# Kernel tuning notes

Hardware: AMD Instinct MI355X
Metric: run time of the kernel (lower is better)

The kernel has to match this reference:

```python
import jax, jax.numpy as jnp
import numpy as np

NUM_CONTEXT = 8  # context panels; +1 choice -> 9 panels, 72 ordered pairs (i != j)

_PAIRS = np.array([(i, j) for i in range(9) for j in range(9) if i != j], dtype=np.int32)
I_IDX = jnp.asarray(_PAIRS[:, 0])  # [72]
J_IDX = jnp.asarray(_PAIRS[:, 1])  # [72]


def setup_inputs() -> dict:
    key = jax.random.key(0)
    ks = jax.random.split(key, 10)
    B, C, F, H = 256, 8, 512, 256
    s_in = 1.0 / np.sqrt(2 * F)
    s_h = 1.0 / np.sqrt(H)
    return {
        "context_features": jax.random.normal(ks[0], (B, NUM_CONTEXT, F), jnp.float32),
        "choice_features": jax.random.normal(ks[1], (B, C, F), jnp.float32),
        "W1": jax.random.uniform(ks[2], (2 * F, H), jnp.float32, -s_in, s_in),
        "b1": jax.random.uniform(ks[3], (H,), jnp.float32, -s_in, s_in),
        "W2": jax.random.uniform(ks[4], (H, H), jnp.float32, -s_h, s_h),
        "b2": jax.random.uniform(ks[5], (H,), jnp.float32, -s_h, s_h),
        "W3": jax.random.uniform(ks[6], (H, H), jnp.float32, -s_h, s_h),
        "b3": jax.random.uniform(ks[7], (H,), jnp.float32, -s_h, s_h),
        "W4": jax.random.uniform(ks[8], (H, 1), jnp.float32, -s_h, s_h),
        "b4": jax.random.uniform(ks[9], (1,), jnp.float32, -s_h, s_h),
    }


def reference(context_features, choice_features, W1, b1, W2, b2, W3, b3, W4, b4):
    B, C, F = choice_features.shape[0], choice_features.shape[1], choice_features.shape[2]
    # panels[b, c, p, f]: 8 context panels + 1 choice panel per candidate choice
    ctx = jnp.broadcast_to(context_features[:, None, :, :], (B, C, NUM_CONTEXT, F))
    panels = jnp.concatenate([ctx, choice_features[:, :, None, :]], axis=2)  # [B,C,9,F]
    # all 72 ordered pairs (i != j), concatenated features -> [B,C,72,2F]
    pair = jnp.concatenate([panels[:, :, I_IDX, :], panels[:, :, J_IDX, :]], axis=-1)
    # g_theta MLP
    h = jax.nn.relu(pair @ W1 + b1)
    h = jax.nn.relu(h @ W2 + b2)        # [B,C,72,H]
    agg = h.mean(axis=2)                # [B,C,H]
    # f_phi MLP (dropout is identity in eval mode)
    g = jax.nn.relu(agg @ W3 + b3)
    score = g @ W4 + b4                 # [B,C,1]
    return score[..., 0]                # [B,C]
```

## Files before the change

kernel.cpp:

```cpp
#include <hip/hip_runtime.h>
#include <hip/hip_bf16.h>


typedef __bf16 bf16_t;
typedef bf16_t bf16x8 __attribute__((ext_vector_type(8)));
typedef bf16_t bf16x4 __attribute__((ext_vector_type(4)));
typedef float f32x4 __attribute__((ext_vector_type(4)));

#define MFMA16(a, b, c) __builtin_amdgcn_mfma_f32_16x16x32_bf16((a), (b), (c), 0, 0, 0)

__global__ __launch_bounds__(256) void prep_kernel(
    const float* __restrict__ W1, const float* __restrict__ W2,
    const float* __restrict__ W3, bf16_t* __restrict__ Wp,
    bf16_t* __restrict__ W2T, bf16_t* __restrict__ W3T) {
  __shared__ float Ts[64][65];
  const int b = blockIdx.x;
  const int t = threadIdx.x;
  const int r = t >> 6;
  const int c = t & 63;
  const float* srcP;
  bf16_t* dstP;
  int srcRow, srcCol, dr0, dc0, dstride;
  if (b < 64) {
    const int k0 = (b >> 3) * 64, j0 = (b & 7) * 64;
    srcP = W1; dstP = Wp; dstride = 512;
    srcRow = (j0 < 256) ? k0 : 512 + k0;
    srcCol = (j0 < 256) ? j0 : j0 - 256;
    dr0 = j0; dc0 = k0;
  } else if (b < 80) {
    const int s = b - 64;
    const int k0 = (s >> 2) * 64, n0 = (s & 3) * 64;
    srcP = W2; dstP = W2T; dstride = 256;
    srcRow = k0; srcCol = n0; dr0 = n0; dc0 = k0;
  } else {
    const int s = b - 80;
    const int k0 = (s >> 2) * 64, n0 = (s & 3) * 64;
    srcP = W3; dstP = W3T; dstride = 256;
    srcRow = k0; srcCol = n0; dr0 = n0; dc0 = k0;
  }
  for (int i = 0; i < 16; ++i) {
    const int a = i * 4 + r;
    Ts[a][c] = srcP[(size_t)(srcRow + a) * 256 + srcCol + c];
  }
  __syncthreads();
  for (int i = 0; i < 16; ++i) {
    const int j = i * 4 + r;
    dstP[(size_t)(dr0 + j) * dstride + dc0 + c] = (bf16_t)Ts[c][j];
  }
}

__global__ __launch_bounds__(512) void k1_kernel(
    const float* __restrict__ ctx, const float* __restrict__ cho,
    const bf16_t* __restrict__ Wp, bf16_t* __restrict__ UV) {
  __shared__ bf16_t As[64][264];
  const int bm = blockIdx.x & 63;
  const int bn = blockIdx.x >> 6;
  const int t = threadIdx.x;
  const int lane = t & 63;
  const int w = t >> 6;
  const int col = lane & 15;
  const int quad = lane >> 4;
  const int n = bn * 128 + w * 16 + col;
  const int sr = t >> 3;
  const int gr = bm * 64 + sr;
  const int bi = gr >> 4;
  const int p = gr & 15;
  const float* src = (p < 8) ? ctx + (size_t)(bi * 8 + p) * 512
                             : cho + (size_t)(bi * 8 + (p - 8)) * 512;
  const int cb = (t & 7) * 4;
  f32x4 acc[4] = {};
  for (int half = 0; half < 2; ++half) {
    const int kbase = half * 256;
    for (int i = 0; i < 8; ++i) {
      const int c = cb + i * 32;
      const f32x4 x = *(const f32x4*)(src + kbase + c);
      bf16x4 y;
      for (int e = 0; e < 4; ++e) y[e] = (bf16_t)x[e];
      *(bf16x4*)(&As[sr][c]) = y;
    }
    __syncthreads();
    for (int ks = 0; ks < 8; ++ks) {
      const int k = ks * 32 + quad * 8;
      bf16x8 af[4];
      for (int mt = 0; mt < 4; ++mt)
        af[mt] = *(const bf16x8*)(&As[mt * 16 + col][k]);
      const bf16x8 bf = *(const bf16x8*)(Wp + (size_t)n * 512 + kbase + k);
      for (int mt = 0; mt < 4; ++mt) acc[mt] = MFMA16(af[mt], bf, acc[mt]);
    }
    __syncthreads();
  }
  for (int mt = 0; mt < 4; ++mt)
    for (int reg = 0; reg < 4; ++reg) {
      const int r = bm * 64 + mt * 16 + quad * 4 + reg;
      UV[(size_t)r * 512 + n] = (bf16_t)acc[mt][reg];
    }
}

__global__ __launch_bounds__(512) void k2_kernel(
    const bf16_t* __restrict__ UV, const float* __restrict__ b1,
    const float* __restrict__ b2, const bf16_t* __restrict__ W2T,
    const bf16_t* __restrict__ W3T, const float* __restrict__ b3,
    const float* __restrict__ W4, const float* __restrict__ b4,
    float* __restrict__ out) {
  __shared__ char smem[138496];
  bf16_t (*UVs)[520] = (bf16_t(*)[520])smem;
  bf16_t (*h1)[136]  = (bf16_t(*)[136])(smem + 16640);
  bf16_t (*W2s)[136] = (bf16_t(*)[136])(smem + 68864);
  float  (*S)[256]   = (float(*)[256])smem;
  bf16_t (*Ag)[264]  = (bf16_t(*)[264])(smem + 16640);
  float  (*red)[8]   = (float(*)[8])(smem + 16640 + 8448);
  const int b = blockIdx.x;
  const int t = threadIdx.x;
  const int lane = t & 63;
  const int w = t >> 6;
  const int col = lane & 15;
  const int quad = lane >> 4;

  {
    const int row = t >> 5;
    const int c0 = (t & 31) * 16;
    const bf16_t* src = UV + (size_t)(b * 16 + row) * 512 + c0;
    *(bf16x8*)(&UVs[row][c0]) = *(const bf16x8*)(src);
    *(bf16x8*)(&UVs[row][c0 + 8]) = *(const bf16x8*)(src + 8);
  }
  const bf16_t* su = nullptr;
  const bf16_t* sv = nullptr;
  int sr = 0, sc0 = 0;
  if (t < 384) {
    sr = t >> 1;
    sc0 = (t & 1) * 64;
    if (sr < 56) {
      const int i = sr / 7;
      const int jj = sr - i * 7;
      const int j = jj + (jj >= i ? 1 : 0);
      su = UVs[i];
      sv = UVs[j] + 256;
    } else if (sr >= 64) {
      const int ch = (sr - 64) >> 4;
      const int rr = (sr - 64) & 15;
      if (rr < 8) { su = UVs[8 + ch]; sv = UVs[rr] + 256; }
      else        { su = UVs[rr - 8]; sv = UVs[8 + ch] + 256; }
    }
  }
  __syncthreads();

  const int mtb = (w & 1) * 6;
  const int q = w >> 1;
  f32x4 acc[6][4] = {};
  for (int half = 0; half < 2; ++half) {
    const int kbase = half * 128;
    if (t < 384) {
      if (su) {
        for (int c = sc0; c < sc0 + 64; c += 8) {
          const bf16x8 u8 = *(const bf16x8*)(su + kbase + c);
          const bf16x8 v8 = *(const bf16x8*)(sv + kbase + c);
          const f32x4 bb0 = *(const f32x4*)(b1 + kbase + c);
          const f32x4 bb1 = *(const f32x4*)(b1 + kbase + c + 4);
          bf16x8 y;
          for (int e = 0; e < 4; ++e)
            y[e] = (bf16_t)fmaxf((float)u8[e] + (float)v8[e] + bb0[e], 0.0f);
          for (int e = 0; e < 4; ++e)
            y[4 + e] = (bf16_t)fmaxf((float)u8[4 + e] + (float)v8[4 + e] + bb1[e], 0.0f);
          *(bf16x8*)(&h1[sr][c]) = y;
        }
      } else if (half == 0) {
        for (int c = sc0; c < sc0 + 64; c += 8)
          *(bf16x8*)(&h1[sr][c]) = (bf16x8)0.0f;
      }
    } else {
      const int n0 = (t - 384) * 2;
      for (int rr = 0; rr < 2; ++rr) {
        const bf16_t* srcw = W2T + (size_t)(n0 + rr) * 256 + kbase;
        for (int cc = 0; cc < 128; cc += 8)
          *(bf16x8*)(&W2s[n0 + rr][cc]) = *(const bf16x8*)(srcw + cc);
      }
    }
    __syncthreads();
    for (int ks = 0; ks < 4; ++ks) {
      const int k = ks * 32 + quad * 8;
      bf16x8 af[6], bfr[4];
      for (int mt = 0; mt < 6; ++mt)
        af[mt] = *(const bf16x8*)(&h1[(mtb + mt) * 16 + col][k]);
      for (int nt = 0; nt < 4; ++nt) {
        const int n = q * 64 + nt * 16 + col;
        bfr[nt] = *(const bf16x8*)(&W2s[n][k]);
      }
      for (int mt = 0; mt < 6; ++mt)
        for (int nt = 0; nt < 4; ++nt)
          acc[mt][nt] = MFMA16(af[mt], bfr[nt], acc[mt][nt]);
    }
    __syncthreads();
  }
  for (int nt = 0; nt < 4; ++nt) {
    const int n = q * 64 + nt * 16 + col;
    const float b2c = b2[n];
    float sctx = 0.0f;
    for (int mt = 0; mt < 6; ++mt) {
      const int gm = mtb + mt;
      float s = 0.0f;
      for (int reg = 0; reg < 4; ++reg) {
        const int row = gm * 16 + quad * 4 + reg;
        if (row < 56 || row >= 64) s += fmaxf(acc[mt][nt][reg] + b2c, 0.0f);
      }
      s += __shfl_xor(s, 16);
      s += __shfl_xor(s, 32);
      if (gm < 4) {
        sctx += s;
      } else if (lane < 16) {
        S[1 + (gm - 4)][n] = s;
      }
    }
    if (mtb == 0 && lane < 16) S[0][n] = sctx;
  }
  __syncthreads();
  {
    const int ch = t >> 6;
    const int n0 = (t & 63) * 4;
    bf16x4 y;
    for (int e = 0; e < 4; ++e)
      y[e] = (bf16_t)((S[0][n0 + e] + S[1 + ch][n0 + e]) * (1.0f / 72.0f));
    *(bf16x4*)(&Ag[ch][n0]) = y;
    *(bf16x4*)(&Ag[8 + ch][n0]) = (bf16x4)0.0f;
  }
  __syncthreads();
  f32x4 acc2[2] = {};
  for (int ks = 0; ks < 8; ++ks) {
    const int k = ks * 32 + quad * 8;
    const bf16x8 af = *(const bf16x8*)(&Ag[col][k]);
    for (int nt = 0; nt < 2; ++nt) {
      const int n = w * 32 + nt * 16 + col;
      const bf16x8 bfr = *(const bf16x8*)(W3T + (size_t)n * 256 + k);
      acc2[nt] = MFMA16(af, bfr, acc2[nt]);
    }
  }
  for (int reg = 0; reg < 4; ++reg) {
    float pr = 0.0f;
    for (int nt = 0; nt < 2; ++nt) {
      const int n = w * 32 + nt * 16 + col;
      pr += fmaxf(acc2[nt][reg] + b3[n], 0.0f) * W4[n];
    }
    pr += __shfl_xor(pr, 1);
    pr += __shfl_xor(pr, 2);
    pr += __shfl_xor(pr, 4);
    pr += __shfl_xor(pr, 8);
    if (col == 0 && quad < 2) red[w][quad * 4 + reg] = pr;
  }
  __syncthreads();
  if (t < 8) {
    float sc = b4[0];
    for (int ww = 0; ww < 8; ++ww) sc += red[ww][t];
    out[b * 8 + t] = sc;
  }
}

extern "C" void kernel_launch(void* const* d_in, const int* in_sizes, int n_in,
                              void* d_out, int out_size, void* d_ws, size_t ws_size,
                              hipStream_t stream) {
  (void)in_sizes; (void)n_in; (void)out_size; (void)ws_size;
  const float* ctx = (const float*)d_in[0];
  const float* cho = (const float*)d_in[1];
  const float* W1  = (const float*)d_in[2];
  const float* b1  = (const float*)d_in[3];
  const float* W2  = (const float*)d_in[4];
  const float* b2  = (const float*)d_in[5];
  const float* W3  = (const float*)d_in[6];
  const float* b3  = (const float*)d_in[7];
  const float* W4  = (const float*)d_in[8];
  const float* b4  = (const float*)d_in[9];
  char* ws = (char*)d_ws;
  bf16_t* Wp   = (bf16_t*)(ws + 0);
  bf16_t* W2T  = (bf16_t*)(ws + 524288);
  bf16_t* W3T  = (bf16_t*)(ws + 655360);
  bf16_t* UV   = (bf16_t*)(ws + 786432);
  float*  out  = (float*)d_out;

  prep_kernel<<<dim3(96), dim3(256), 0, stream>>>(W1, W2, W3, Wp, W2T, W3T);
  k1_kernel<<<dim3(256), dim3(512), 0, stream>>>(ctx, cho, Wp, UV);
  k2_kernel<<<dim3(256), dim3(512), 0, stream>>>(UV, b1, b2, W2T, W3T, b3, W4, b4, out);
}
```

Measured before the change: 105.2 us.

## Fuse weight prep into first GEMM kernel with global flag synchronization

Merges the weight transpose/convert kernel and the first GEMM kernel into one launch. The first 96 blocks convert the weights and bump a global atomic counter. The GEMM blocks stage their first activation half into LDS and then spin until all weights are ready. The counter is reset at the end of the second kernel. This removes one launch and overlaps activation loading with weight conversion, but it depends on the prep blocks being scheduled before or alongside the waiting blocks, which risks deadlock or spin overhead.

```diff
diff --git a/kernel.cpp b/kernel.cpp
--- a/kernel.cpp
+++ b/kernel.cpp
@@ -9,53 +9,61 @@
 
 #define MFMA16(a, b, c) __builtin_amdgcn_mfma_f32_16x16x32_bf16((a), (b), (c), 0, 0, 0)
 
-__global__ __launch_bounds__(256) void prep_kernel(
+__device__ int g_flag = 0;
+
+__global__ __launch_bounds__(512, 4) void k01_kernel(
+    const float* __restrict__ ctx, const float* __restrict__ cho,
     const float* __restrict__ W1, const float* __restrict__ W2,
     const float* __restrict__ W3, bf16_t* __restrict__ Wp,
-    bf16_t* __restrict__ W2T, bf16_t* __restrict__ W3T) {
-  __shared__ float Ts[64][65];
-  const int b = blockIdx.x;
+    bf16_t* __restrict__ W2T, bf16_t* __restrict__ W3T,
+    bf16_t* __restrict__ UV) {
+  __shared__ char smem[33792];
   const int t = threadIdx.x;
-  const int r = t >> 6;
-  const int c = t & 63;
-  const float* srcP;
-  bf16_t* dstP;
-  int srcRow, srcCol, dr0, dc0, dstride;
-  if (b < 64) {
-    const int k0 = (b >> 3) * 64, j0 = (b & 7) * 64;
-    srcP = W1; dstP = Wp; dstride = 512;
-    srcRow = (j0 < 256) ? k0 : 512 + k0;
-    srcCol = (j0 < 256) ? j0 : j0 - 256;
-    dr0 = j0; dc0 = k0;
-  } else if (b < 80) {
-    const int s = b - 64;
-    const int k0 = (s >> 2) * 64, n0 = (s & 3) * 64;
-    srcP = W2; dstP = W2T; dstride = 256;
-    srcRow = k0; srcCol = n0; dr0 = n0; dc0 = k0;
-  } else {
-    const int s = b - 80;
-    const int k0 = (s >> 2) * 64, n0 = (s & 3) * 64;
-    srcP = W3; dstP = W3T; dstride = 256;
-    srcRow = k0; srcCol = n0; dr0 = n0; dc0 = k0;
-  }
-  for (int i = 0; i < 16; ++i) {
-    const int a = i * 4 + r;
-    Ts[a][c] = srcP[(size_t)(srcRow + a) * 256 + srcCol + c];
-  }
-  __syncthreads();
-  for (int i = 0; i < 16; ++i) {
-    const int j = i * 4 + r;
-    dstP[(size_t)(dr0 + j) * dstride + dc0 + c] = (bf16_t)Ts[c][j];
-  }
-}
-
-__global__ __launch_bounds__(512) void k1_kernel(
-    const float* __restrict__ ctx, const float* __restrict__ cho,
-    const bf16_t* __restrict__ Wp, bf16_t* __restrict__ UV) {
-  __shared__ bf16_t As[64][264];
-  const int bm = blockIdx.x & 63;
-  const int bn = blockIdx.x >> 6;
-  const int t = threadIdx.x;
+
+  if (blockIdx.x < 96) {
+    float (*Ts)[65] = (float(*)[65])smem;
+    const int b = blockIdx.x;
+    const int r = t >> 6;
+    const int c = t & 63;
+    const float* srcP;
+    bf16_t* dstP;
+    int srcRow, srcCol, dr0, dc0, dstride;
+    if (b < 64) {
+      const int k0 = (b >> 3) * 64, j0 = (b & 7) * 64;
+      srcP = W1; dstP = Wp; dstride = 512;
+      srcRow = (j0 < 256) ? k0 : 512 + k0;
+      srcCol = (j0 < 256) ? j0 : j0 - 256;
+      dr0 = j0; dc0 = k0;
+    } else if (b < 80) {
+      const int s = b - 64;
+      const int k0 = (s >> 2) * 64, n0 = (s & 3) * 64;
+      srcP = W2; dstP = W2T; dstride = 256;
+      srcRow = k0; srcCol = n0; dr0 = n0; dc0 = k0;
+    } else {
+      const int s = b - 80;
+      const int k0 = (s >> 2) * 64, n0 = (s & 3) * 64;
+      srcP = W3; dstP = W3T; dstride = 256;
+      srcRow = k0; srcCol = n0; dr0 = n0; dc0 = k0;
+    }
+    for (int i = 0; i < 8; ++i) {
+      const int a = i * 8 + r;
+      Ts[a][c] = srcP[(size_t)(srcRow + a) * 256 + srcCol + c];
+    }
+    __syncthreads();
+    for (int i = 0; i < 8; ++i) {
+      const int j = i * 8 + r;
+      dstP[(size_t)(dr0 + j) * dstride + dc0 + c] = (bf16_t)Ts[c][j];
+    }
+    __threadfence();
+    __syncthreads();
+    if (t == 0) atomicAdd(&g_flag, 1);
+    return;
+  }
+
+  bf16_t (*As)[264] = (bf16_t(*)[264])smem;
+  const int bid = blockIdx.x - 96;
+  const int bm = bid & 63;
+  const int bn = bid >> 6;
   const int lane = t & 63;
   const int w = t >> 6;
   const int col = lane & 15;
@@ -68,17 +76,33 @@
   const float* src = (p < 8) ? ctx + (size_t)(bi * 8 + p) * 512
                              : cho + (size_t)(bi * 8 + (p - 8)) * 512;
   const int cb = (t & 7) * 4;
+
+  for (int i = 0; i < 8; ++i) {
+    const int c = cb + i * 32;
+    const f32x4 x = *(const f32x4*)(src + c);
+    bf16x4 y;
+    for (int e = 0; e < 4; ++e) y[e] = (bf16_t)x[e];
+    *(bf16x4*)(&As[sr][c]) = y;
+  }
+  if (t == 0) {
+    while (atomicAdd(&g_flag, 0) < 96) __builtin_amdgcn_s_sleep(2);
+  }
+  __syncthreads();
+  __threadfence();
+
   f32x4 acc[4] = {};
   for (int half = 0; half < 2; ++half) {
     const int kbase = half * 256;
-    for (int i = 0; i < 8; ++i) {
-      const int c = cb + i * 32;
-      const f32x4 x = *(const f32x4*)(src + kbase + c);
-      bf16x4 y;
-      for (int e = 0; e < 4; ++e) y[e] = (bf16_t)x[e];
-      *(bf16x4*)(&As[sr][c]) = y;
-    }
-    __syncthreads();
+    if (half == 1) {
+      for (int i = 0; i < 8; ++i) {
+        const int c = cb + i * 32;
+        const f32x4 x = *(const f32x4*)(src + kbase + c);
+        bf16x4 y;
+        for (int e = 0; e < 4; ++e) y[e] = (bf16_t)x[e];
+        *(bf16x4*)(&As[sr][c]) = y;
+      }
+      __syncthreads();
+    }
     for (int ks = 0; ks < 8; ++ks) {
       const int k = ks * 32 + quad * 8;
       bf16x8 af[4];
@@ -251,6 +275,7 @@
     for (int ww = 0; ww < 8; ++ww) sc += red[ww][t];
     out[b * 8 + t] = sc;
   }
+  if (b == 0 && t == 0) atomicExch(&g_flag, 0);
 }
 
 extern "C" void kernel_launch(void* const* d_in, const int* in_sizes, int n_in,
@@ -274,7 +299,8 @@
   bf16_t* UV   = (bf16_t*)(ws + 786432);
   float*  out  = (float*)d_out;
 
-  prep_kernel<<<dim3(96), dim3(256), 0, stream>>>(W1, W2, W3, Wp, W2T, W3T);
-  k1_kernel<<<dim3(256), dim3(512), 0, stream>>>(ctx, cho, Wp, UV);
-  k2_kernel<<<dim3(256), dim3(512), 0, stream>>>(UV, b1, b2, W2T, W3T, b3, W4, b4, out);
+  k01_kernel<<<dim3(352), dim3(512), 0, stream>>>(ctx, cho, W1, W2, W3,
+                                                  Wp, W2T, W3T, UV);
+  k2_kernel<<<dim3(256), dim3(512), 0, stream>>>(UV, b1, b2, W2T, W3T, b3,
+                                                 W4, b4, out);
 }
```

New measurement: 156.0 us. +48.2%, slower.
